# Kernel optimization log

Measured on AMD Instinct MI355X. Metric: run time of the kernel, lower is better.

Reference implementation:

```python
import jax, jax.numpy as jnp
import numpy as np

B, A, F, S = 8192, 128, 16, 8

def setup_inputs() -> dict:
    key = jax.random.key(0)
    k1, k2, k3, k4 = jax.random.split(key, 4)
    c_iso = jax.random.normal(k1, (B, A, F), dtype=jnp.float32)
    int_iso = jax.random.uniform(k2, (B, A, F), dtype=jnp.float32)
    segment = jax.random.randint(k3, (B, A), 0, S, dtype=jnp.int64)
    charges = jax.random.normal(k4, (B, S), dtype=jnp.float32)
    return {"c_iso": c_iso, "int_iso": int_iso, "segment": segment, "charges": charges}

def reference(c_iso, int_iso, segment, charges):
    # c_iso, int_iso: [B, A, F]; segment: [B, A] in [0, S); charges: [B, S]
    b, a, f = c_iso.shape
    s = charges.shape[1]
    # global segment id per atom, flattened over batch (as in torch segment_r)
    seg_flat = (jnp.arange(b, dtype=segment.dtype)[:, None] * s + segment).reshape(-1)  # [B*A]
    c = c_iso.reshape(-1, f)   # [B*A, F]
    q = int_iso.reshape(-1, f)  # [B*A, F]
    nseg = b * s
    # KKT system [[2I, q],[-q^T, 0]] x = [2c; -charge] per segment has closed form
    # x = c - q * (q.c - charge) / (q.q)
    qc = jax.ops.segment_sum(jnp.sum(c * q, axis=-1), seg_flat, num_segments=nseg)  # [B*S]
    qq = jax.ops.segment_sum(jnp.sum(q * q, axis=-1), seg_flat, num_segments=nseg)  # [B*S]
    lam = (qc - charges.reshape(-1)) / qq  # [B*S] (half the Lagrange multiplier)
    x = c - q * lam[seg_flat][:, None]
    return x.reshape(b, a, f)
```

## Files before the change

kernel.cpp:

```cpp
#include <hip/hip_runtime.h>
#include <hip/hip_bf16.h>


#define B_ 8192
#define A_ 128
#define F_ 16
#define S_ 8

#define WPB 4
#define VPB (A_ * F_ / 4)
#define VPL (VPB / 64)

__global__ __launch_bounds__(64 * WPB) void qp_seg_norm_kernel(
    const float* __restrict__ c_iso,
    const float* __restrict__ int_iso,
    const int*   __restrict__ segment,
    const float* __restrict__ charges,
    float*       __restrict__ out)
{
    const int w    = threadIdx.x >> 6;
    const int lane = threadIdx.x & 63;
    const int b    = blockIdx.x * WPB + w;

    float charge = 0.0f;
    if (lane < S_) charge = charges[(size_t)b * S_ + lane];

    const float4* cp = reinterpret_cast<const float4*>(c_iso)   + (size_t)b * VPB;
    const float4* qp = reinterpret_cast<const float4*>(int_iso) + (size_t)b * VPB;
    const int*    sp = segment + (size_t)b * A_;

    float4 cv[VPL], qv[VPL];
    unsigned sgp = 0;

#pragma unroll
    for (int j = 0; j < VPL; ++j) {
        const int v = j * 64 + lane;
        cv[j] = cp[v];
        qv[j] = qp[v];
        sgp |= ((unsigned)sp[v >> 2]) << (4 * j);
    }

    float aqc[S_], aqq[S_];
#pragma unroll
    for (int s = 0; s < S_; ++s) { aqc[s] = 0.0f; aqq[s] = 0.0f; }

#pragma unroll
    for (int j = 0; j < VPL; ++j) {
        const float cq = cv[j].x * qv[j].x + cv[j].y * qv[j].y
                       + cv[j].z * qv[j].z + cv[j].w * qv[j].w;
        const float qq = qv[j].x * qv[j].x + qv[j].y * qv[j].y
                       + qv[j].z * qv[j].z + qv[j].w * qv[j].w;
        const int sj = (int)((sgp >> (4 * j)) & 7u);
#pragma unroll
        for (int s = 0; s < S_; ++s) {
            const bool m = (sj == s);
            aqc[s] += m ? cq : 0.0f;
            aqq[s] += m ? qq : 0.0f;
        }
    }

#pragma unroll
    for (int m = 1; m < 64; m <<= 1) {
#pragma unroll
        for (int s = 0; s < S_; ++s) {
            aqc[s] += __shfl_xor(aqc[s], m, 64);
            aqq[s] += __shfl_xor(aqq[s], m, 64);
        }
    }

    float qcsel = aqc[0], qqsel = aqq[0];
#pragma unroll
    for (int s = 1; s < S_; ++s) {
        const bool m = (lane == s);
        qcsel = m ? aqc[s] : qcsel;
        qqsel = m ? aqq[s] : qqsel;
    }
    const float lamv = (qcsel - charge) / qqsel;

    float4* op = reinterpret_cast<float4*>(out) + (size_t)b * VPB;
#pragma unroll
    for (int j = 0; j < VPL; ++j) {
        const int sj = (int)((sgp >> (4 * j)) & 7u);
        const float lam = __shfl(lamv, sj, 64);
        const int v = j * 64 + lane;
        float4 r;
        r.x = cv[j].x - qv[j].x * lam;
        r.y = cv[j].y - qv[j].y * lam;
        r.z = cv[j].z - qv[j].z * lam;
        r.w = cv[j].w - qv[j].w * lam;
        op[v] = r;
    }
}

extern "C" void kernel_launch(void* const* d_in, const int* in_sizes, int n_in,
                              void* d_out, int out_size, void* d_ws, size_t ws_size,
                              hipStream_t stream) {
    const float* c_iso   = (const float*)d_in[0];
    const float* int_iso = (const float*)d_in[1];
    const int*   segment = (const int*)d_in[2];
    const float* charges = (const float*)d_in[3];
    float* out = (float*)d_out;

    qp_seg_norm_kernel<<<B_ / WPB, 64 * WPB, 0, stream>>>(
        c_iso, int_iso, segment, charges, out);
}
```

Before: 36.09 us.

## Use recursive-halving transpose reduction for segment sums and nontemporal output stores

Replaces the full butterfly reduction of 16 per-segment partial sums across 64 lanes with a recursive-halving scheme. Each step exchanges half the values and keeps the half selected by the lane bit, which cuts the number of cross-lane shuffles from 96 to about 32. A lookup table maps each segment to the lane that holds its lambda. Output stores become nontemporal to avoid cache pollution. The cost is a more intricate lane-to-segment mapping, with charges loaded by every lane.

```diff
diff --git a/kernel.cpp b/kernel.cpp
--- a/kernel.cpp
+++ b/kernel.cpp
@@ -11,6 +11,8 @@
 #define VPB (A_ * F_ / 4)
 #define VPL (VPB / 64)
 
+typedef float f4 __attribute__((ext_vector_type(4)));
+
 __global__ __launch_bounds__(64 * WPB) void qp_seg_norm_kernel(
     const float* __restrict__ c_iso,
     const float* __restrict__ int_iso,
@@ -22,14 +24,14 @@
     const int lane = threadIdx.x & 63;
     const int b    = blockIdx.x * WPB + w;
 
-    float charge = 0.0f;
-    if (lane < S_) charge = charges[(size_t)b * S_ + lane];
+    const int sl = ((lane >> 1) & 1) * 4 + ((lane >> 2) & 1) * 2 + ((lane >> 3) & 1);
+    const float charge = charges[(size_t)b * S_ + sl];
 
-    const float4* cp = reinterpret_cast<const float4*>(c_iso)   + (size_t)b * VPB;
-    const float4* qp = reinterpret_cast<const float4*>(int_iso) + (size_t)b * VPB;
-    const int*    sp = segment + (size_t)b * A_;
+    const f4* cp = reinterpret_cast<const f4*>(c_iso)   + (size_t)b * VPB;
+    const f4* qp = reinterpret_cast<const f4*>(int_iso) + (size_t)b * VPB;
+    const int* sp = segment + (size_t)b * A_;
 
-    float4 cv[VPL], qv[VPL];
+    f4 cv[VPL], qv[VPL];
     unsigned sgp = 0;
 
 #pragma unroll
@@ -40,9 +42,9 @@
         sgp |= ((unsigned)sp[v >> 2]) << (4 * j);
     }
 
-    float aqc[S_], aqq[S_];
+    float val[16];
 #pragma unroll
-    for (int s = 0; s < S_; ++s) { aqc[s] = 0.0f; aqq[s] = 0.0f; }
+    for (int k = 0; k < 16; ++k) val[k] = 0.0f;
 
 #pragma unroll
     for (int j = 0; j < VPL; ++j) {
@@ -54,41 +56,50 @@
 #pragma unroll
         for (int s = 0; s < S_; ++s) {
             const bool m = (sj == s);
-            aqc[s] += m ? cq : 0.0f;
-            aqq[s] += m ? qq : 0.0f;
+            val[s]      += m ? cq : 0.0f;
+            val[8 + s]  += m ? qq : 0.0f;
         }
     }
 
 #pragma unroll
-    for (int m = 1; m < 64; m <<= 1) {
+    for (int k = 0; k < 16; ++k) val[k] += __shfl_xor(val[k], 1, 64);
+    float v8[8];
 #pragma unroll
-        for (int s = 0; s < S_; ++s) {
-            aqc[s] += __shfl_xor(aqc[s], m, 64);
-            aqq[s] += __shfl_xor(aqq[s], m, 64);
-        }
-    }
+    for (int k = 0; k < 8; ++k) v8[k] = (lane & 1) ? val[8 + k] : val[k];
+#pragma unroll
+    for (int k = 0; k < 8; ++k) v8[k] += __shfl_xor(v8[k], 2, 64);
+    float v4a[4];
+#pragma unroll
+    for (int k = 0; k < 4; ++k) v4a[k] = (lane & 2) ? v8[4 + k] : v8[k];
+#pragma unroll
+    for (int k = 0; k < 4; ++k) v4a[k] += __shfl_xor(v4a[k], 4, 64);
+    float v2a[2];
+#pragma unroll
+    for (int k = 0; k < 2; ++k) v2a[k] = (lane & 4) ? v4a[2 + k] : v4a[k];
+#pragma unroll
+    for (int k = 0; k < 2; ++k) v2a[k] += __shfl_xor(v2a[k], 8, 64);
+    float v1 = (lane & 8) ? v2a[1] : v2a[0];
+    v1 += __shfl_xor(v1, 16, 64);
+    v1 += __shfl_xor(v1, 32, 64);
 
-    float qcsel = aqc[0], qqsel = aqq[0];
-#pragma unroll
-    for (int s = 1; s < S_; ++s) {
-        const bool m = (lane == s);
-        qcsel = m ? aqc[s] : qcsel;
-        qqsel = m ? aqq[s] : qqsel;
-    }
-    const float lamv = (qcsel - charge) / qqsel;
+    const float prt = __shfl_xor(v1, 1, 64);
+    const float lamv = (v1 - charge) / prt;
 
-    float4* op = reinterpret_cast<float4*>(out) + (size_t)b * VPB;
+    const unsigned Ltab = 0xE6A2C480u;
+
+    f4* op = reinterpret_cast<f4*>(out) + (size_t)b * VPB;
 #pragma unroll
     for (int j = 0; j < VPL; ++j) {
         const int sj = (int)((sgp >> (4 * j)) & 7u);
-        const float lam = __shfl(lamv, sj, 64);
+        const int src = (int)((Ltab >> (4 * sj)) & 15u);
+        const float lam = __shfl(lamv, src, 64);
         const int v = j * 64 + lane;
-        float4 r;
+        f4 r;
         r.x = cv[j].x - qv[j].x * lam;
         r.y = cv[j].y - qv[j].y * lam;
         r.z = cv[j].z - qv[j].z * lam;
         r.w = cv[j].w - qv[j].w * lam;
-        op[v] = r;
+        __builtin_nontemporal_store(r, op + v);
     }
 }
 
```

Measured after the change: 42.46 us. +17.7%, slower.
